# Performance work log

Hardware: AMD Instinct MI355X
Metric: run time of the kernel (lower is better)

Reference implementation:

```python
import jax, jax.numpy as jnp
import numpy as np

B, EMBED, HEADS, T = 2, 512, 8, 2048
DH = EMBED // HEADS
EPS = 1e-5
# NOTE: torch code computes embed_dim // num_heads ** 0.5 == 512 // sqrt(8)
SCALE = EMBED // HEADS ** 0.5  # = 181.0, reproduced faithfully


def ws_conv1x1(x, w, b, mask):
    # weight-standardized 1x1 conv; w: [O, I], x: [B, I, T], mask: [B, T]
    mu = jnp.mean(w, axis=1, keepdims=True)
    var = jnp.var(w, axis=1, keepdims=True)
    wn = (w - mu) * jax.lax.rsqrt(var + EPS)
    x = x * mask[:, None, :].astype(x.dtype)
    return jnp.einsum('oi,bit->bot', wn, x) + b[None, :, None]


def ln_head(x, g, b):
    # per-head LayerNorm over head dim; x: [B, H, DH, T], normalized over DH
    xt = jnp.swapaxes(x, -1, -2)  # [B, H, T, DH]
    mu = jnp.mean(xt, axis=-1, keepdims=True)
    var = jnp.var(xt, axis=-1, keepdims=True)
    xn = (xt - mu) * jax.lax.rsqrt(var + EPS) * g + b
    return jnp.swapaxes(xn, -1, -2)


def setup_inputs():
    key = jax.random.key(0)
    ks = jax.random.split(key, 12)
    sc = 1.0 / np.sqrt(EMBED)
    d = {
        'q': jax.random.normal(ks[0], (B, EMBED, T), jnp.float32),
        'k': jax.random.normal(ks[1], (B, EMBED, T), jnp.float32),
        'v': jax.random.normal(ks[2], (B, EMBED, T), jnp.float32),
        'query_mask': jax.random.randint(ks[3], (B, T), 0, 2, jnp.int32),
        'key_mask': jax.random.randint(ks[4], (B, T), 0, 2, jnp.int32),
        'value_mask': jax.random.randint(ks[5], (B, T), 0, 2, jnp.int32),
        'Wq': jax.random.normal(ks[6], (EMBED, EMBED), jnp.float32) * sc,
        'bq': jnp.zeros((EMBED,), jnp.float32),
        'Wk': jax.random.normal(ks[7], (EMBED, EMBED), jnp.float32) * sc,
        'bk': jnp.zeros((EMBED,), jnp.float32),
        'Wv': jax.random.normal(ks[8], (EMBED, EMBED), jnp.float32) * sc,
        'bv': jnp.zeros((EMBED,), jnp.float32),
        'Wo': jax.random.normal(ks[9], (EMBED, EMBED), jnp.float32) * sc,
        'bo': jnp.zeros((EMBED,), jnp.float32),
        'ln_gq': jnp.ones((DH,), jnp.float32), 'ln_bq': jnp.zeros((DH,), jnp.float32),
        'ln_gk': jnp.ones((DH,), jnp.float32), 'ln_bk': jnp.zeros((DH,), jnp.float32),
        'ln_gv': jnp.ones((DH,), jnp.float32), 'ln_bv': jnp.zeros((DH,), jnp.float32),
    }
    return d


def reference(q, k, v, query_mask, key_mask, value_mask,
              Wq, bq, Wk, bk, Wv, bv, Wo, bo,
              ln_gq, ln_bq, ln_gk, ln_bk, ln_gv, ln_bv):
    q = ws_conv1x1(q, Wq, bq, query_mask)   # [B, E, T]
    k = ws_conv1x1(k, Wk, bk, key_mask)
    v = ws_conv1x1(v, Wv, bv, value_mask)
    # split heads: [B, E, T] -> [B, H, DH, T]
    q = q.reshape(B, HEADS, DH, T)
    k = k.reshape(B, HEADS, DH, T)
    v = v.reshape(B, HEADS, DH, T)
    # middle_norm: per-head LayerNorm over DH
    q = ln_head(q, ln_gq, ln_bq)
    k = ln_head(k, ln_gk, ln_bk)
    v = ln_head(v, ln_gv, ln_bv)
    # scores = q^T k / scale : [B, H, Tq, Tk]
    scores = jnp.einsum('bhdq,bhdk->bhqk', q, k) / SCALE
    scores = jnp.where(key_mask[:, None, None, :] == 0, -1e9, scores)
    scores = jax.nn.softmax(scores, axis=-1)
    scores = jnp.where(query_mask[:, None, :, None] == 0, 0.0, scores)
    # out = (scores @ v^T)^T : [B, H, DH, Tq]
    out = jnp.einsum('bhqk,bhdk->bhdq', scores, v)
    out = out.reshape(B, EMBED, T)
    out = ws_conv1x1(out, Wo, bo, query_mask)
    return out
```

## Files before the change

### kernel.cpp

```cpp
#include <hip/hip_runtime.h>


typedef __bf16 bf16;
typedef __bf16 bf16x8 __attribute__((ext_vector_type(8)));
typedef float  f32x4  __attribute__((ext_vector_type(4)));

#define MFMA_BF16(a, b, c) __builtin_amdgcn_mfma_f32_16x16x32_bf16((a), (b), (c), 0, 0, 0)

#define NB   2
#define NE   512
#define NH   8
#define NT   2048
#define NDH  64

__device__ __forceinline__ void gl_lds16(const bf16* g, bf16* l) {
  __builtin_amdgcn_global_load_lds(
      (const __attribute__((address_space(1))) void*)g,
      (__attribute__((address_space(3))) void*)l, 16, 0, 0);
}

__global__ __launch_bounds__(64) void k_wstd(
    const float* __restrict__ Wq, const float* __restrict__ Wk,
    const float* __restrict__ Wv, const float* __restrict__ Wo,
    bf16* __restrict__ out)
{
  const float* W = blockIdx.y == 0 ? Wq : blockIdx.y == 1 ? Wk
                 : blockIdx.y == 2 ? Wv : Wo;
  int row = blockIdx.x, lane = threadIdx.x;
  const float4* p = (const float4*)(W + row * NE) + lane * 2;
  float4 a = p[0], c = p[1];
  float s  = a.x + a.y + a.z + a.w + c.x + c.y + c.z + c.w;
  float ss = a.x*a.x + a.y*a.y + a.z*a.z + a.w*a.w
           + c.x*c.x + c.y*c.y + c.z*c.z + c.w*c.w;
#pragma unroll
  for (int m = 1; m < 64; m <<= 1) { s += __shfl_xor(s, m); ss += __shfl_xor(ss, m); }
  float mean = s * (1.0f / NE);
  float var  = ss * (1.0f / NE) - mean * mean;
  float rstd = rsqrtf(var + 1e-5f);
  bf16x8 o;
  o[0] = (bf16)((a.x - mean) * rstd); o[1] = (bf16)((a.y - mean) * rstd);
  o[2] = (bf16)((a.z - mean) * rstd); o[3] = (bf16)((a.w - mean) * rstd);
  o[4] = (bf16)((c.x - mean) * rstd); o[5] = (bf16)((c.y - mean) * rstd);
  o[6] = (bf16)((c.z - mean) * rstd); o[7] = (bf16)((c.w - mean) * rstd);
  *(bf16x8*)(out + blockIdx.y * (NE * NE) + row * NE + lane * 8) = o;
}

__global__ __launch_bounds__(256) void k_trans(
    const float* __restrict__ q, const float* __restrict__ k,
    const float* __restrict__ v,
    const int* __restrict__ qm, const int* __restrict__ km,
    const int* __restrict__ vm,
    bf16* __restrict__ xT)
{
  int src = blockIdx.z >> 1, b = blockIdx.z & 1;
  const float* x = src == 0 ? q : src == 1 ? k : v;
  const int*   m = src == 0 ? qm : src == 1 ? km : vm;
  x += (size_t)b * NE * NT;
  m += b * NT;
  int t0 = blockIdx.x * 64, i0 = blockIdx.y * 64;
  __shared__ float tile[64][65];
  int tt = threadIdx.x & 63, ii = threadIdx.x >> 6;
#pragma unroll
  for (int i = ii; i < 64; i += 4)
    tile[i][tt] = x[(size_t)(i0 + i) * NT + t0 + tt];
  __syncthreads();
  bf16* o = xT + ((size_t)src * NB + b) * NT * NE;
  int i2 = threadIdx.x & 63, t2 = threadIdx.x >> 6;
#pragma unroll
  for (int t = t2; t < 64; t += 4) {
    float mk = (float)m[t0 + t];
    o[(size_t)(t0 + t) * NE + i0 + i2] = (bf16)(tile[i2][t] * mk);
  }
}

__global__ __launch_bounds__(256) void k_proj(
    const bf16* __restrict__ Wn,
    const bf16* __restrict__ xT,
    const float* __restrict__ bq, const float* __restrict__ bk,
    const float* __restrict__ bv,
    const float* __restrict__ gq, const float* __restrict__ bbq,
    const float* __restrict__ gk, const float* __restrict__ bbk,
    const float* __restrict__ gv, const float* __restrict__ bbv,
    bf16* __restrict__ Qh, bf16* __restrict__ Kh, bf16* __restrict__ Vh)
{
  int src = blockIdx.z >> 1, b = blockIdx.z & 1;
  const bf16* A  = Wn + src * (NE * NE);
  const bf16* Bm = xT + ((size_t)src * NB + b) * NT * NE;
  int m0 = blockIdx.y * 64, n0 = blockIdx.x * 128;
  int h = m0 >> 6;

  __shared__ __align__(16) char smem[64 * 129 * 4 + 2 * 128 * 4];
  bf16*  Al = (bf16*)smem;
  bf16*  Bl = (bf16*)(smem + 8192);
  float* Yl = (float*)smem;
  float* mu = (float*)(smem + 64 * 129 * 4);
  float* rs = mu + 128;

  int tid = threadIdx.x, lane = tid & 63, w = tid >> 6;
  int mh = (w & 1) * 32, nh = (w >> 1) * 64;
  f32x4 acc[2][4] = {};

  for (int k0 = 0; k0 < NE; k0 += 64) {
    __syncthreads();
#pragma unroll
    for (int i = 0; i < 2; i++) {
      int row = (w << 4) + (i << 3) + (lane >> 3);
      int chg = (lane & 7) ^ (row & 7);
      gl_lds16(A + (m0 + row) * NE + k0 + (chg << 3),
               Al + ((w << 4) + (i << 3)) * 64);
    }
#pragma unroll
    for (int i = 0; i < 4; i++) {
      int row = (w << 5) + (i << 3) + (lane >> 3);
      int chg = (lane & 7) ^ (row & 7);
      gl_lds16(Bm + (size_t)(n0 + row) * NE + k0 + (chg << 3),
               Bl + ((w << 5) + (i << 3)) * 64);
    }
    __syncthreads();
#pragma unroll
    for (int kk = 0; kk < 64; kk += 32) {
      bf16x8 af[2], bfv[4];
#pragma unroll
      for (int ms = 0; ms < 2; ms++) {
        int row = mh + ms * 16 + (lane & 15);
        af[ms] = *(const bf16x8*)(Al + row * 64 +
                   ((((kk >> 3) + (lane >> 4)) ^ (row & 7)) << 3));
      }
#pragma unroll
      for (int ns = 0; ns < 4; ns++) {
        int row = nh + ns * 16 + (lane & 15);
        bfv[ns] = *(const bf16x8*)(Bl + row * 64 +
                   ((((kk >> 3) + (lane >> 4)) ^ (row & 7)) << 3));
      }
#pragma unroll
      for (int ms = 0; ms < 2; ms++)
#pragma unroll
        for (int ns = 0; ns < 4; ns++)
          acc[ms][ns] = MFMA_BF16(af[ms], bfv[ns], acc[ms][ns]);
    }
  }

  __syncthreads();
  {
    const float* bias = src == 0 ? bq : src == 1 ? bk : bv;
#pragma unroll
    for (int ms = 0; ms < 2; ms++)
#pragma unroll
      for (int ns = 0; ns < 4; ns++)
#pragma unroll
        for (int r = 0; r < 4; r++) {
          int om = mh + ms * 16 + ((lane >> 4) << 2) + r;
          int on = nh + ns * 16 + (lane & 15);
          Yl[om * 129 + on] = acc[ms][ns][r] + bias[m0 + om];
        }
  }
  __syncthreads();
  if (tid < 128) {
    float s = 0.f, ss = 0.f;
#pragma unroll 8
    for (int o = 0; o < 64; o++) { float y = Yl[o * 129 + tid]; s += y; ss += y * y; }
    float mean = s * (1.0f / 64.0f);
    float var  = ss * (1.0f / 64.0f) - mean * mean;
    mu[tid] = mean;
    rs[tid] = rsqrtf(var + 1e-5f);
  }
  __syncthreads();

  if (src < 2) {
    float scl = (src == 0) ? (1.0f / 181.0f) : 1.0f;
    const float* g  = src == 0 ? gq  : gk;
    const float* bb = src == 0 ? bbq : bbk;
    bf16* out = (src == 0 ? Qh : Kh) + ((size_t)(b * NH + h) * NT + n0) * NDH;
    int d = tid & 63, tb = tid >> 6;
    float gg = g[d] * scl, bb2 = bb[d] * scl;
#pragma unroll
    for (int t = tb; t < 128; t += 4) {
      float val = (Yl[d * 129 + t] - mu[t]) * rs[t] * gg + bb2;
      out[(size_t)t * NDH + d] = (bf16)val;
    }
  } else {
    bf16* out = Vh + (size_t)(b * NH + h) * NDH * NT + n0;
    int t = tid & 127, db = tid >> 7;
#pragma unroll
    for (int d = db; d < 64; d += 2) {
      float val = (Yl[d * 129 + t] - mu[t]) * rs[t] * gv[d] + bbv[d];
      out[(size_t)d * NT + t] = (bf16)val;
    }
  }
}

__global__ __launch_bounds__(256, 2) void k_attn(
    const bf16* __restrict__ Qh, const bf16* __restrict__ Kh,
    const bf16* __restrict__ Vh,
    const int* __restrict__ qmask, const int* __restrict__ kmask,
    bf16* __restrict__ xa)
{
  int bh = blockIdx.y, b = bh >> 3, h = bh & 7;
  int q0 = blockIdx.x * 64;
  const bf16* Q = Qh + (size_t)bh * NT * NDH;
  const bf16* K = Kh + (size_t)bh * NT * NDH;
  const bf16* V = Vh + (size_t)bh * NDH * NT;

  __shared__ __align__(16) char smem[2 * 64 * 68 * 4 + 4 * 64 * 4];
  float* OlA  = (float*)smem;
  float* OlB  = (float*)(smem + 64 * 68 * 4);
  float* denl = (float*)(smem + 2 * 64 * 68 * 4);

  int tid = threadIdx.x, lane = tid & 63, w = tid >> 6;
  int quad = lane >> 4, l15 = lane & 15;
  bf16* Plw = (bf16*)smem + w * (64 * 40);

  bf16x8 aq[4][2];
#pragma unroll
  for (int qs = 0; qs < 4; qs++)
#pragma unroll
    for (int hf = 0; hf < 2; hf++)
      aq[qs][hf] = *(const bf16x8*)(Q + (size_t)(q0 + qs * 16 + l15) * NDH + hf * 32 + quad * 8);

  f32x4 acco[4][4] = {};
  float den[4][4] = {};

  const int ko = w * 32;
  const bf16* Kbase = K + (size_t)ko * NDH + quad * 8;
  const bf16* Vbase = V + (size_t)l15 * NT + ko + quad * 8;

  bf16x8 kb00, kb01, kb10, kb11, vb0, vb1, vb2, vb3;
  {
    const bf16* kp = Kbase + (size_t)l15 * NDH;
    kb00 = *(const bf16x8*)(kp);             kb01 = *(const bf16x8*)(kp + 32);
    kb10 = *(const bf16x8*)(kp + 16 * NDH);  kb11 = *(const bf16x8*)(kp + 16 * NDH + 32);
    vb0 = *(const bf16x8*)(Vbase);
    vb1 = *(const bf16x8*)(Vbase + 16 * NT);
    vb2 = *(const bf16x8*)(Vbase + 32 * NT);
    vb3 = *(const bf16x8*)(Vbase + 48 * NT);
  }

  for (int k0 = 0; k0 < NT; k0 += 128) {
    int k1 = (k0 + 128) & (NT - 1);
    bf16x8 n00, n01, n10, n11, nv0, nv1, nv2, nv3;
    {
      const bf16* kp = Kbase + (size_t)(k1 + l15) * NDH;
      n00 = *(const bf16x8*)(kp);             n01 = *(const bf16x8*)(kp + 32);
      n10 = *(const bf16x8*)(kp + 16 * NDH);  n11 = *(const bf16x8*)(kp + 16 * NDH + 32);
      const bf16* vp = Vbase + k1;
      nv0 = *(const bf16x8*)(vp);
      nv1 = *(const bf16x8*)(vp + 16 * NT);
      nv2 = *(const bf16x8*)(vp + 32 * NT);
      nv3 = *(const bf16x8*)(vp + 48 * NT);
    }
    float km0 = (float)kmask[b * NT + k0 + ko + l15];
    float km1 = (float)kmask[b * NT + k0 + ko + 16 + l15];

    f32x4 s[4][2];
#pragma unroll
    for (int qs = 0; qs < 4; qs++) {
      f32x4 z0 = {}; z0 = MFMA_BF16(aq[qs][0], kb00, z0); z0 = MFMA_BF16(aq[qs][1], kb01, z0); s[qs][0] = z0;
      f32x4 z1 = {}; z1 = MFMA_BF16(aq[qs][0], kb10, z1); z1 = MFMA_BF16(aq[qs][1], kb11, z1); s[qs][1] = z1;
    }
#pragma unroll
    for (int qs = 0; qs < 4; qs++)
#pragma unroll
      for (int n = 0; n < 2; n++) {
        float km = n ? km1 : km0;
#pragma unroll
        for (int r = 0; r < 4; r++) {
          float p = __expf(s[qs][n][r]) * km;
          den[qs][r] += p;
          Plw[(qs * 16 + quad * 4 + r) * 40 + n * 16 + l15] = (bf16)p;
        }
      }
#pragma unroll
    for (int qs = 0; qs < 4; qs++) {
      bf16x8 pa = *(const bf16x8*)(Plw + (qs * 16 + l15) * 40 + quad * 8);
      acco[qs][0] = MFMA_BF16(pa, vb0, acco[qs][0]);
      acco[qs][1] = MFMA_BF16(pa, vb1, acco[qs][1]);
      acco[qs][2] = MFMA_BF16(pa, vb2, acco[qs][2]);
      acco[qs][3] = MFMA_BF16(pa, vb3, acco[qs][3]);
    }
    kb00 = n00; kb01 = n01; kb10 = n10; kb11 = n11;
    vb0 = nv0; vb1 = nv1; vb2 = nv2; vb3 = nv3;
  }

#pragma unroll
  for (int m = 1; m < 16; m <<= 1)
#pragma unroll
    for (int qs = 0; qs < 4; qs++)
#pragma unroll
      for (int r = 0; r < 4; r++)
        den[qs][r] += __shfl_xor(den[qs][r], m);

  __syncthreads();
  if (l15 == 0)
#pragma unroll
    for (int qs = 0; qs < 4; qs++)
#pragma unroll
      for (int r = 0; r < 4; r++)
        denl[w * 64 + qs * 16 + quad * 4 + r] = den[qs][r];

  float* Obuf = (w < 2) ? OlA : OlB;
  if ((w & 1) == 0) {
#pragma unroll
    for (int qs = 0; qs < 4; qs++)
#pragma unroll
      for (int ds = 0; ds < 4; ds++)
#pragma unroll
        for (int r = 0; r < 4; r++)
          Obuf[(qs * 16 + quad * 4 + r) * 68 + ds * 16 + l15] = acco[qs][ds][r];
  }
  __syncthreads();
  if (w & 1) {
#pragma unroll
    for (int qs = 0; qs < 4; qs++)
#pragma unroll
      for (int ds = 0; ds < 4; ds++)
#pragma unroll
        for (int r = 0; r < 4; r++)
          Obuf[(qs * 16 + quad * 4 + r) * 68 + ds * 16 + l15] += acco[qs][ds][r];
  }
  __syncthreads();

#pragma unroll
  for (int i = 0; i < 16; i++) {
    int ql = w * 16 + i;
    float dtot = denl[ql] + denl[64 + ql] + denl[128 + ql] + denl[192 + ql];
    float qm = (float)qmask[b * NT + q0 + ql];
    float inv = qm / dtot;
    float val = (OlA[ql * 68 + lane] + OlB[ql * 68 + lane]) * inv;
    xa[((size_t)b * NT + q0 + ql) * NE + h * NDH + lane] = (bf16)val;
  }
}

__global__ __launch_bounds__(256) void k_oproj(
    const bf16* __restrict__ A,
    const bf16* __restrict__ xab,
    const float* __restrict__ bo, float* __restrict__ out)
{
  int b = blockIdx.z;
  const bf16* Bm = xab + (size_t)b * NT * NE;
  int m0 = blockIdx.y * 64, n0 = blockIdx.x * 128;

  __shared__ __align__(16) char smem[24576];
  bf16* Al = (bf16*)smem;
  bf16* Bl = (bf16*)(smem + 8192);

  int tid = threadIdx.x, lane = tid & 63, w = tid >> 6;
  int mh = (w & 1) * 32, nh = (w >> 1) * 64;
  f32x4 acc[2][4] = {};

  for (int k0 = 0; k0 < NE; k0 += 64) {
    __syncthreads();
#pragma unroll
    for (int i = 0; i < 2; i++) {
      int row = (w << 4) + (i << 3) + (lane >> 3);
      int chg = (lane & 7) ^ (row & 7);
      gl_lds16(A + (m0 + row) * NE + k0 + (chg << 3),
               Al + ((w << 4) + (i << 3)) * 64);
    }
#pragma unroll
    for (int i = 0; i < 4; i++) {
      int row = (w << 5) + (i << 3) + (lane >> 3);
      int chg = (lane & 7) ^ (row & 7);
      gl_lds16(Bm + (size_t)(n0 + row) * NE + k0 + (chg << 3),
               Bl + ((w << 5) + (i << 3)) * 64);
    }
    __syncthreads();
#pragma unroll
    for (int kk = 0; kk < 64; kk += 32) {
      bf16x8 af[2], bfv[4];
#pragma unroll
      for (int ms = 0; ms < 2; ms++) {
        int row = mh + ms * 16 + (lane & 15);
        af[ms] = *(const bf16x8*)(Al + row * 64 +
                   ((((kk >> 3) + (lane >> 4)) ^ (row & 7)) << 3));
      }
#pragma unroll
      for (int ns = 0; ns < 4; ns++) {
        int row = nh + ns * 16 + (lane & 15);
        bfv[ns] = *(const bf16x8*)(Bl + row * 64 +
                   ((((kk >> 3) + (lane >> 4)) ^ (row & 7)) << 3));
      }
#pragma unroll
      for (int ms = 0; ms < 2; ms++)
#pragma unroll
        for (int ns = 0; ns < 4; ns++)
          acc[ms][ns] = MFMA_BF16(af[ms], bfv[ns], acc[ms][ns]);
    }
  }

#pragma unroll
  for (int ms = 0; ms < 2; ms++)
#pragma unroll
    for (int ns = 0; ns < 4; ns++)
#pragma unroll
      for (int r = 0; r < 4; r++) {
        int o = m0 + mh + ms * 16 + ((lane >> 4) << 2) + r;
        int t = n0 + nh + ns * 16 + (lane & 15);
        out[(size_t)b * NE * NT + (size_t)o * NT + t] = acc[ms][ns][r] + bo[o];
      }
}

extern "C" void kernel_launch(void* const* d_in, const int* in_sizes, int n_in,
                              void* d_out, int out_size, void* d_ws, size_t ws_size,
                              hipStream_t stream)
{
  const float* q  = (const float*)d_in[0];
  const float* k  = (const float*)d_in[1];
  const float* v  = (const float*)d_in[2];
  const int*   qm = (const int*)d_in[3];
  const int*   km = (const int*)d_in[4];
  const int*   vm = (const int*)d_in[5];
  const float* Wq = (const float*)d_in[6];  const float* bq = (const float*)d_in[7];
  const float* Wk = (const float*)d_in[8];  const float* bk = (const float*)d_in[9];
  const float* Wv = (const float*)d_in[10]; const float* bv = (const float*)d_in[11];
  const float* Wo = (const float*)d_in[12]; const float* bo = (const float*)d_in[13];
  const float* gq = (const float*)d_in[14]; const float* bbq = (const float*)d_in[15];
  const float* gk = (const float*)d_in[16]; const float* bbk = (const float*)d_in[17];
  const float* gv = (const float*)d_in[18]; const float* bbv = (const float*)d_in[19];
  float* out = (float*)d_out;

  char* wsb = (char*)d_ws;
  bf16* Wn  = (bf16*)(wsb);
  bf16* xT  = (bf16*)(wsb + (2ull  << 20));
  bf16* Qh  = (bf16*)(wsb + (14ull << 20));
  bf16* Kh  = (bf16*)(wsb + (18ull << 20));
  bf16* Vh  = (bf16*)(wsb + (22ull << 20));
  bf16* xa  = (bf16*)(wsb + (26ull << 20));

  k_wstd <<<dim3(512, 4),   64,  0, stream>>>(Wq, Wk, Wv, Wo, Wn);
  k_trans<<<dim3(32, 8, 6), 256, 0, stream>>>(q, k, v, qm, km, vm, xT);
  k_proj <<<dim3(16, 8, 6), 256, 0, stream>>>(Wn, xT, bq, bk, bv,
                                              gq, bbq, gk, bbk, gv, bbv,
                                              Qh, Kh, Vh);
  k_attn <<<dim3(32, 16),   256, 0, stream>>>(Qh, Kh, Vh, qm, km, xa);
  k_oproj<<<dim3(16, 8, 2), 256, 0, stream>>>(Wn + 3 * NE * NE, xa, bo, out);
}
```

Baseline: 178.5 us.

## Keep attention probabilities in registers via transposed QK and f16 PV MFMA

The attention kernel computes S^T by swapping MFMA operands, so each lane's score fragment already matches the A-operand layout of a 16x16x16 f16 MFMA. Probabilities therefore go straight from registers into the PV product, with no LDS round trip through a per-wave P buffer. V is now stored as f16 and the key mask is pre-converted to floats by an extra block row in the weight-standardization kernel, so it can be read as float4. Separately, the output projection tile shrinks to 64x64 to double the block count, and the projection's LDS row stride goes from 129 to 130 floats. The trade-offs are twice as many K16 MFMAs for PV, f16 range limits on exp(scores) and V, and an extra small workspace buffer.

```diff
diff --git a/kernel.cpp b/kernel.cpp
--- a/kernel.cpp
+++ b/kernel.cpp
@@ -3,9 +3,12 @@
 
 typedef __bf16 bf16;
 typedef __bf16 bf16x8 __attribute__((ext_vector_type(8)));
+typedef _Float16 f16;
+typedef _Float16 f16x4 __attribute__((ext_vector_type(4)));
 typedef float  f32x4  __attribute__((ext_vector_type(4)));
 
 #define MFMA_BF16(a, b, c) __builtin_amdgcn_mfma_f32_16x16x32_bf16((a), (b), (c), 0, 0, 0)
+#define MFMA_F16_K16(a, b, c) __builtin_amdgcn_mfma_f32_16x16x16f16((a), (b), (c), 0, 0, 0)
 
 #define NB   2
 #define NE   512
@@ -22,8 +25,14 @@
 __global__ __launch_bounds__(64) void k_wstd(
     const float* __restrict__ Wq, const float* __restrict__ Wk,
     const float* __restrict__ Wv, const float* __restrict__ Wo,
-    bf16* __restrict__ out)
-{
+    const int* __restrict__ km,
+    bf16* __restrict__ out, float* __restrict__ kmf)
+{
+  if (blockIdx.y == 4) {
+    int idx = blockIdx.x * 64 + threadIdx.x;
+    if (idx < NB * NT) kmf[idx] = (float)km[idx];
+    return;
+  }
   const float* W = blockIdx.y == 0 ? Wq : blockIdx.y == 1 ? Wk
                  : blockIdx.y == 2 ? Wv : Wo;
   int row = blockIdx.x, lane = threadIdx.x;
@@ -81,7 +90,7 @@
     const float* __restrict__ gq, const float* __restrict__ bbq,
     const float* __restrict__ gk, const float* __restrict__ bbk,
     const float* __restrict__ gv, const float* __restrict__ bbv,
-    bf16* __restrict__ Qh, bf16* __restrict__ Kh, bf16* __restrict__ Vh)
+    bf16* __restrict__ Qh, bf16* __restrict__ Kh, f16* __restrict__ Vh)
 {
   int src = blockIdx.z >> 1, b = blockIdx.z & 1;
   const bf16* A  = Wn + src * (NE * NE);
@@ -89,11 +98,11 @@
   int m0 = blockIdx.y * 64, n0 = blockIdx.x * 128;
   int h = m0 >> 6;
 
-  __shared__ __align__(16) char smem[64 * 129 * 4 + 2 * 128 * 4];
+  __shared__ __align__(16) char smem[64 * 130 * 4 + 2 * 128 * 4];
   bf16*  Al = (bf16*)smem;
   bf16*  Bl = (bf16*)(smem + 8192);
   float* Yl = (float*)smem;
-  float* mu = (float*)(smem + 64 * 129 * 4);
+  float* mu = (float*)(smem + 64 * 130 * 4);
   float* rs = mu + 128;
 
   int tid = threadIdx.x, lane = tid & 63, w = tid >> 6;
@@ -151,14 +160,14 @@
         for (int r = 0; r < 4; r++) {
           int om = mh + ms * 16 + ((lane >> 4) << 2) + r;
           int on = nh + ns * 16 + (lane & 15);
-          Yl[om * 129 + on] = acc[ms][ns][r] + bias[m0 + om];
+          Yl[om * 130 + on] = acc[ms][ns][r] + bias[m0 + om];
         }
   }
   __syncthreads();
   if (tid < 128) {
     float s = 0.f, ss = 0.f;
 #pragma unroll 8
-    for (int o = 0; o < 64; o++) { float y = Yl[o * 129 + tid]; s += y; ss += y * y; }
+    for (int o = 0; o < 64; o++) { float y = Yl[o * 130 + tid]; s += y; ss += y * y; }
     float mean = s * (1.0f / 64.0f);
     float var  = ss * (1.0f / 64.0f) - mean * mean;
     mu[tid] = mean;
@@ -175,31 +184,31 @@
     float gg = g[d] * scl, bb2 = bb[d] * scl;
 #pragma unroll
     for (int t = tb; t < 128; t += 4) {
-      float val = (Yl[d * 129 + t] - mu[t]) * rs[t] * gg + bb2;
+      float val = (Yl[d * 130 + t] - mu[t]) * rs[t] * gg + bb2;
       out[(size_t)t * NDH + d] = (bf16)val;
     }
   } else {
-    bf16* out = Vh + (size_t)(b * NH + h) * NDH * NT + n0;
+    f16* out = Vh + (size_t)(b * NH + h) * NDH * NT + n0;
     int t = tid & 127, db = tid >> 7;
 #pragma unroll
     for (int d = db; d < 64; d += 2) {
-      float val = (Yl[d * 129 + t] - mu[t]) * rs[t] * gv[d] + bbv[d];
-      out[(size_t)d * NT + t] = (bf16)val;
+      float val = (Yl[d * 130 + t] - mu[t]) * rs[t] * gv[d] + bbv[d];
+      out[(size_t)d * NT + t] = (f16)val;
     }
   }
 }
 
 __global__ __launch_bounds__(256, 2) void k_attn(
     const bf16* __restrict__ Qh, const bf16* __restrict__ Kh,
-    const bf16* __restrict__ Vh,
-    const int* __restrict__ qmask, const int* __restrict__ kmask,
+    const f16* __restrict__ Vh,
+    const float* __restrict__ kmf, const int* __restrict__ qmask,
     bf16* __restrict__ xa)
 {
   int bh = blockIdx.y, b = bh >> 3, h = bh & 7;
   int q0 = blockIdx.x * 64;
   const bf16* Q = Qh + (size_t)bh * NT * NDH;
   const bf16* K = Kh + (size_t)bh * NT * NDH;
-  const bf16* V = Vh + (size_t)bh * NDH * NT;
+  const f16*  V = Vh + (size_t)bh * NDH * NT;
 
   __shared__ __align__(16) char smem[2 * 64 * 68 * 4 + 4 * 64 * 4];
   float* OlA  = (float*)smem;
@@ -208,94 +217,103 @@
 
   int tid = threadIdx.x, lane = tid & 63, w = tid >> 6;
   int quad = lane >> 4, l15 = lane & 15;
-  bf16* Plw = (bf16*)smem + w * (64 * 40);
-
-  bf16x8 aq[4][2];
+  const int ko = w * 32;
+
+  bf16x8 qb[4][2];
 #pragma unroll
   for (int qs = 0; qs < 4; qs++)
 #pragma unroll
     for (int hf = 0; hf < 2; hf++)
-      aq[qs][hf] = *(const bf16x8*)(Q + (size_t)(q0 + qs * 16 + l15) * NDH + hf * 32 + quad * 8);
+      qb[qs][hf] = *(const bf16x8*)(Q + (size_t)(q0 + qs * 16 + l15) * NDH + hf * 32 + quad * 8);
+
+  const bf16*  Kb = K + (size_t)(ko + l15) * NDH + quad * 8;
+  const f16*   Vb = V + (size_t)l15 * NT + ko + quad * 4;
+  const float* Mb = kmf + b * NT + ko + quad * 4;
 
   f32x4 acco[4][4] = {};
-  float den[4][4] = {};
-
-  const int ko = w * 32;
-  const bf16* Kbase = K + (size_t)ko * NDH + quad * 8;
-  const bf16* Vbase = V + (size_t)l15 * NT + ko + quad * 8;
-
-  bf16x8 kb00, kb01, kb10, kb11, vb0, vb1, vb2, vb3;
-  {
-    const bf16* kp = Kbase + (size_t)l15 * NDH;
-    kb00 = *(const bf16x8*)(kp);             kb01 = *(const bf16x8*)(kp + 32);
-    kb10 = *(const bf16x8*)(kp + 16 * NDH);  kb11 = *(const bf16x8*)(kp + 16 * NDH + 32);
-    vb0 = *(const bf16x8*)(Vbase);
-    vb1 = *(const bf16x8*)(Vbase + 16 * NT);
-    vb2 = *(const bf16x8*)(Vbase + 32 * NT);
-    vb3 = *(const bf16x8*)(Vbase + 48 * NT);
-  }
+  float den[4] = {};
+
+  bf16x8 ka[2][2];
+  f16x4  vb[4][2];
+#pragma unroll
+  for (int kt = 0; kt < 2; kt++)
+#pragma unroll
+    for (int hf = 0; hf < 2; hf++)
+      ka[kt][hf] = *(const bf16x8*)(Kb + (size_t)(kt * 16) * NDH + hf * 32);
+#pragma unroll
+  for (int ds = 0; ds < 4; ds++)
+#pragma unroll
+    for (int kt = 0; kt < 2; kt++)
+      vb[ds][kt] = *(const f16x4*)(Vb + (size_t)(ds * 16) * NT + kt * 16);
 
   for (int k0 = 0; k0 < NT; k0 += 128) {
     int k1 = (k0 + 128) & (NT - 1);
-    bf16x8 n00, n01, n10, n11, nv0, nv1, nv2, nv3;
-    {
-      const bf16* kp = Kbase + (size_t)(k1 + l15) * NDH;
-      n00 = *(const bf16x8*)(kp);             n01 = *(const bf16x8*)(kp + 32);
-      n10 = *(const bf16x8*)(kp + 16 * NDH);  n11 = *(const bf16x8*)(kp + 16 * NDH + 32);
-      const bf16* vp = Vbase + k1;
-      nv0 = *(const bf16x8*)(vp);
-      nv1 = *(const bf16x8*)(vp + 16 * NT);
-      nv2 = *(const bf16x8*)(vp + 32 * NT);
-      nv3 = *(const bf16x8*)(vp + 48 * NT);
-    }
-    float km0 = (float)kmask[b * NT + k0 + ko + l15];
-    float km1 = (float)kmask[b * NT + k0 + ko + 16 + l15];
-
-    f32x4 s[4][2];
-#pragma unroll
-    for (int qs = 0; qs < 4; qs++) {
-      f32x4 z0 = {}; z0 = MFMA_BF16(aq[qs][0], kb00, z0); z0 = MFMA_BF16(aq[qs][1], kb01, z0); s[qs][0] = z0;
-      f32x4 z1 = {}; z1 = MFMA_BF16(aq[qs][0], kb10, z1); z1 = MFMA_BF16(aq[qs][1], kb11, z1); s[qs][1] = z1;
-    }
+    bf16x8 nka[2][2];
+    f16x4  nvb[4][2];
+#pragma unroll
+    for (int kt = 0; kt < 2; kt++)
+#pragma unroll
+      for (int hf = 0; hf < 2; hf++)
+        nka[kt][hf] = *(const bf16x8*)(Kb + (size_t)(k1 + kt * 16) * NDH + hf * 32);
+#pragma unroll
+    for (int ds = 0; ds < 4; ds++)
+#pragma unroll
+      for (int kt = 0; kt < 2; kt++)
+        nvb[ds][kt] = *(const f16x4*)(Vb + (size_t)(ds * 16) * NT + k1 + kt * 16);
+
+    float4 kmv0 = *(const float4*)(Mb + k0);
+    float4 kmv1 = *(const float4*)(Mb + k0 + 16);
+
+#pragma unroll
+    for (int kt = 0; kt < 2; kt++) {
+      const float4 kmv = kt ? kmv1 : kmv0;
+      f32x4 s[4];
+#pragma unroll
+      for (int qs = 0; qs < 4; qs++) {
+        f32x4 z = {};
+        z = MFMA_BF16(ka[kt][0], qb[qs][0], z);
+        z = MFMA_BF16(ka[kt][1], qb[qs][1], z);
+        s[qs] = z;
+      }
+      f16x4 pa[4];
+#pragma unroll
+      for (int qs = 0; qs < 4; qs++) {
+        float p0 = __expf(s[qs][0]) * kmv.x;
+        float p1 = __expf(s[qs][1]) * kmv.y;
+        float p2 = __expf(s[qs][2]) * kmv.z;
+        float p3 = __expf(s[qs][3]) * kmv.w;
+        den[qs] += (p0 + p1) + (p2 + p3);
+        f16x4 pv; pv[0] = (f16)p0; pv[1] = (f16)p1; pv[2] = (f16)p2; pv[3] = (f16)p3;
+        pa[qs] = pv;
+      }
+#pragma unroll
+      for (int qs = 0; qs < 4; qs++)
+#pragma unroll
+        for (int ds = 0; ds < 4; ds++)
+          acco[qs][ds] = MFMA_F16_K16(pa[qs], vb[ds][kt], acco[qs][ds]);
+    }
+
+#pragma unroll
+    for (int kt = 0; kt < 2; kt++)
+#pragma unroll
+      for (int hf = 0; hf < 2; hf++)
+        ka[kt][hf] = nka[kt][hf];
+#pragma unroll
+    for (int ds = 0; ds < 4; ds++)
+#pragma unroll
+      for (int kt = 0; kt < 2; kt++)
+        vb[ds][kt] = nvb[ds][kt];
+  }
+
+#pragma unroll
+  for (int qs = 0; qs < 4; qs++) {
+    den[qs] += __shfl_xor(den[qs], 16);
+    den[qs] += __shfl_xor(den[qs], 32);
+  }
+  if (quad == 0)
 #pragma unroll
     for (int qs = 0; qs < 4; qs++)
-#pragma unroll
-      for (int n = 0; n < 2; n++) {
-        float km = n ? km1 : km0;
-#pragma unroll
-        for (int r = 0; r < 4; r++) {
-          float p = __expf(s[qs][n][r]) * km;
-          den[qs][r] += p;
-          Plw[(qs * 16 + quad * 4 + r) * 40 + n * 16 + l15] = (bf16)p;
-        }
-      }
-#pragma unroll
-    for (int qs = 0; qs < 4; qs++) {
-      bf16x8 pa = *(const bf16x8*)(Plw + (qs * 16 + l15) * 40 + quad * 8);
-      acco[qs][0] = MFMA_BF16(pa, vb0, acco[qs][0]);
-      acco[qs][1] = MFMA_BF16(pa, vb1, acco[qs][1]);
-      acco[qs][2] = MFMA_BF16(pa, vb2, acco[qs][2]);
-      acco[qs][3] = MFMA_BF16(pa, vb3, acco[qs][3]);
-    }
-    kb00 = n00; kb01 = n01; kb10 = n10; kb11 = n11;
-    vb0 = nv0; vb1 = nv1; vb2 = nv2; vb3 = nv3;
-  }
-
-#pragma unroll
-  for (int m = 1; m < 16; m <<= 1)
-#pragma unroll
-    for (int qs = 0; qs < 4; qs++)
-#pragma unroll
-      for (int r = 0; r < 4; r++)
-        den[qs][r] += __shfl_xor(den[qs][r], m);
-
-  __syncthreads();
-  if (l15 == 0)
-#pragma unroll
-    for (int qs = 0; qs < 4; qs++)
-#pragma unroll
-      for (int r = 0; r < 4; r++)
-        denl[w * 64 + qs * 16 + quad * 4 + r] = den[qs][r];
+      denl[w * 64 + qs * 16 + l15] = den[qs];
 
   float* Obuf = (w < 2) ? OlA : OlB;
   if ((w & 1) == 0) {
@@ -337,15 +355,15 @@
 {
   int b = blockIdx.z;
   const bf16* Bm = xab + (size_t)b * NT * NE;
-  int m0 = blockIdx.y * 64, n0 = blockIdx.x * 128;
-
-  __shared__ __align__(16) char smem[24576];
+  int m0 = blockIdx.y * 64, n0 = blockIdx.x * 64;
+
+  __shared__ __align__(16) char smem[16384];
   bf16* Al = (bf16*)smem;
   bf16* Bl = (bf16*)(smem + 8192);
 
   int tid = threadIdx.x, lane = tid & 63, w = tid >> 6;
-  int mh = (w & 1) * 32, nh = (w >> 1) * 64;
-  f32x4 acc[2][4] = {};
+  int mh = (w & 1) * 32, nh = (w >> 1) * 32;
+  f32x4 acc[2][2] = {};
 
   for (int k0 = 0; k0 < NE; k0 += 64) {
     __syncthreads();
@@ -357,16 +375,16 @@
                Al + ((w << 4) + (i << 3)) * 64);
     }
 #pragma unroll
-    for (int i = 0; i < 4; i++) {
-      int row = (w << 5) + (i << 3) + (lane >> 3);
+    for (int i = 0; i < 2; i++) {
+      int row = (w << 4) + (i << 3) + (lane >> 3);
       int chg = (lane & 7) ^ (row & 7);
       gl_lds16(Bm + (size_t)(n0 + row) * NE + k0 + (chg << 3),
-               Bl + ((w << 5) + (i << 3)) * 64);
+               Bl + ((w << 4) + (i << 3)) * 64);
     }
     __syncthreads();
 #pragma unroll
     for (int kk = 0; kk < 64; kk += 32) {
-      bf16x8 af[2], bfv[4];
+      bf16x8 af[2], bfv[2];
 #pragma unroll
       for (int ms = 0; ms < 2; ms++) {
         int row = mh + ms * 16 + (lane & 15);
@@ -374,7 +392,7 @@
                    ((((kk >> 3) + (lane >> 4)) ^ (row & 7)) << 3));
       }
 #pragma unroll
-      for (int ns = 0; ns < 4; ns++) {
+      for (int ns = 0; ns < 2; ns++) {
         int row = nh + ns * 16 + (lane & 15);
         bfv[ns] = *(const bf16x8*)(Bl + row * 64 +
                    ((((kk >> 3) + (lane >> 4)) ^ (row & 7)) << 3));
@@ -382,7 +400,7 @@
 #pragma unroll
       for (int ms = 0; ms < 2; ms++)
 #pragma unroll
-        for (int ns = 0; ns < 4; ns++)
+        for (int ns = 0; ns < 2; ns++)
           acc[ms][ns] = MFMA_BF16(af[ms], bfv[ns], acc[ms][ns]);
     }
   }
@@ -390,7 +408,7 @@
 #pragma unroll
   for (int ms = 0; ms < 2; ms++)
 #pragma unroll
-    for (int ns = 0; ns < 4; ns++)
+    for (int ns = 0; ns < 2; ns++)
 #pragma unroll
       for (int r = 0; r < 4; r++) {
         int o = m0 + mh + ms * 16 + ((lane >> 4) << 2) + r;
@@ -419,18 +437,19 @@
   float* out = (float*)d_out;
 
   char* wsb = (char*)d_ws;
-  bf16* Wn  = (bf16*)(wsb);
-  bf16* xT  = (bf16*)(wsb + (2ull  << 20));
-  bf16* Qh  = (bf16*)(wsb + (14ull << 20));
-  bf16* Kh  = (bf16*)(wsb + (18ull << 20));
-  bf16* Vh  = (bf16*)(wsb + (22ull << 20));
-  bf16* xa  = (bf16*)(wsb + (26ull << 20));
-
-  k_wstd <<<dim3(512, 4),   64,  0, stream>>>(Wq, Wk, Wv, Wo, Wn);
+  bf16*  Wn  = (bf16*)(wsb);
+  bf16*  xT  = (bf16*)(wsb + (2ull  << 20));
+  bf16*  Qh  = (bf16*)(wsb + (14ull << 20));
+  bf16*  Kh  = (bf16*)(wsb + (18ull << 20));
+  f16*   Vh  = (f16*) (wsb + (22ull << 20));
+  bf16*  xa  = (bf16*)(wsb + (26ull << 20));
+  float* kmf = (float*)(wsb + (30ull << 20));
+
+  k_wstd <<<dim3(512, 5),   64,  0, stream>>>(Wq, Wk, Wv, Wo, km, Wn, kmf);
   k_trans<<<dim3(32, 8, 6), 256, 0, stream>>>(q, k, v, qm, km, vm, xT);
   k_proj <<<dim3(16, 8, 6), 256, 0, stream>>>(Wn, xT, bq, bk, bv,
                                               gq, bbq, gk, bbk, gv, bbv,
                                               Qh, Kh, Vh);
-  k_attn <<<dim3(32, 16),   256, 0, stream>>>(Qh, Kh, Vh, qm, km, xa);
-  k_oproj<<<dim3(16, 8, 2), 256, 0, stream>>>(Wn + 3 * NE * NE, xa, bo, out);
-}
+  k_attn <<<dim3(32, 16),   256, 0, stream>>>(Qh, Kh, Vh, kmf, qm, xa);
+  k_oproj<<<dim3(32, 8, 2), 256, 0, stream>>>(Wn + 3 * NE * NE, xa, bo, out);
+}
```

Result: slower. 187.8 us (+5.2%).
